# Kernel optimization log

Hardware: AMD Instinct MI355X
Metric: run time of the kernel (lower is better)

Reference implementation:

```python
import jax, jax.numpy as jnp
import numpy as np

N_NODES = 100000
N_EDGES = 1600000
N_GRAPHS = 128
IN_DIM, HID, OUT_DIM, DOC_DIM = 64, 128, 32, 768
LAYERS = 3


def setup_inputs() -> dict:
    key = jax.random.key(0)
    ks = jax.random.split(key, 24)
    s = 0.05
    inp = {
        "x": jax.random.normal(ks[0], (N_NODES, IN_DIM), jnp.float32),
        "doc_features": jax.random.normal(ks[1], (N_GRAPHS, DOC_DIM), jnp.float32),
        "edge_index": jax.random.randint(ks[2], (2, N_EDGES), 0, N_NODES, jnp.int64),
        "batch": jnp.sort(jax.random.randint(ks[3], (N_NODES,), 0, N_GRAPHS, jnp.int64)),
        # parameters (stored as [in, out] so y = x @ W + b)
        "node_w": jax.random.normal(ks[4], (IN_DIM, HID), jnp.float32) * s,
        "node_b": jnp.zeros((HID,), jnp.float32),
        "ggnn_w": jax.random.normal(ks[5], (LAYERS, HID, HID), jnp.float32) * s,
        "gru_w_ih": jax.random.normal(ks[6], (HID, 3 * HID), jnp.float32) * s,
        "gru_b_ih": jnp.zeros((3 * HID,), jnp.float32),
        "gru_w_hh": jax.random.normal(ks[7], (HID, 3 * HID), jnp.float32) * s,
        "gru_b_hh": jnp.zeros((3 * HID,), jnp.float32),
        "doc_w": jax.random.normal(ks[8], (DOC_DIM, HID), jnp.float32) * s,
        "doc_b": jnp.zeros((HID,), jnp.float32),
        "ln_g": jnp.ones((2 * HID,), jnp.float32),
        "ln_b": jnp.zeros((2 * HID,), jnp.float32),
        "fus_w": jax.random.normal(ks[9], (2 * HID, HID), jnp.float32) * s,
        "fus_b": jnp.zeros((HID,), jnp.float32),
        "task_w": jax.random.normal(ks[10], (HID, OUT_DIM), jnp.float32) * s,
        "task_b": jnp.zeros((OUT_DIM,), jnp.float32),
        "time_w": jax.random.normal(ks[11], (HID, 1), jnp.float32) * s,
        "time_b": jnp.zeros((1,), jnp.float32),
    }
    return inp


def _gru(m, h, w_ih, b_ih, w_hh, b_hh):
    gi = m @ w_ih + b_ih  # [N, 3H]
    gh = h @ w_hh + b_hh
    ir, iz, in_ = jnp.split(gi, 3, axis=-1)
    hr, hz, hn = jnp.split(gh, 3, axis=-1)
    r = jax.nn.sigmoid(ir + hr)
    z = jax.nn.sigmoid(iz + hz)
    n = jnp.tanh(in_ + r * hn)
    return (1.0 - z) * n + z * h


def reference(x, doc_features, node_w, node_b, ggnn_w, gru_w_ih, gru_b_ih,
              gru_w_hh, gru_b_hh, doc_w, doc_b, ln_g, ln_b, fus_w, fus_b,
              task_w, task_b, time_w, time_b, edge_index, batch):
    N = x.shape[0]
    src, dst = edge_index[0], edge_index[1]
    # node projection + ReLU
    h = jax.nn.relu(x @ node_w + node_b)  # [N, H]
    # GatedGraphConv: 3 layers of (linear -> scatter-add over edges -> GRU)
    for i in range(LAYERS):
        m = h @ ggnn_w[i]                              # [N, H]
        agg = jax.ops.segment_sum(m[src], dst, num_segments=N)  # scatter-add
        h = _gru(agg, h, gru_w_ih, gru_b_ih, gru_w_hh, gru_b_hh)
    # global mean pool over graphs
    sums = jax.ops.segment_sum(h, batch, num_segments=N_GRAPHS)  # [G, H]
    cnt = jax.ops.segment_sum(jnp.ones((N,), h.dtype), batch, num_segments=N_GRAPHS)
    pooled = sums / jnp.maximum(cnt, 1.0)[:, None]
    # doc projection + fusion head
    doc_emb = jax.nn.relu(doc_features @ doc_w + doc_b)  # [G, H]
    fusion = jnp.concatenate([pooled, doc_emb], axis=1)  # [G, 2H]
    mu = jnp.mean(fusion, axis=-1, keepdims=True)
    var = jnp.mean(jnp.square(fusion - mu), axis=-1, keepdims=True)
    fusion = (fusion - mu) * jax.lax.rsqrt(var + 1e-5) * ln_g + ln_b
    fusion = jax.nn.relu(fusion @ fus_w + fus_b)  # dropout is identity (eval)
    task_output = fusion @ task_w + task_b
    time_output = fusion @ time_w + time_b
    return (task_output, time_output)
```

## Files before the change

### kernel.cpp

```cpp
#include <hip/hip_runtime.h>

#define N_NODES  100000
#define N_EDGES  1600000
#define N_GRAPHS 128

#define BSH      8
#define BNODES   (1 << BSH)
#define NBUCK    391
#define NBLK_P1  512
#define EPB      (N_EDGES / NBLK_P1)
#define BKT_SCAN_N   (NBUCK * NBLK_P1)
#define SCAN_BLK_BKT 196
#define SCAN_BLK_NODE 98

typedef unsigned short u16;
typedef unsigned int   u32;
typedef __attribute__((ext_vector_type(8))) short short8;
typedef __attribute__((ext_vector_type(4))) float f32x4;

__device__ __forceinline__ float bf2f(u16 v) {
  union { u32 i; float f; } u; u.i = ((u32)v) << 16; return u.f;
}
__device__ __forceinline__ u16 f2bf(float f) {
  union { float f; u32 i; } u; u.f = f;
  u32 r = (u.i + 0x7fffu + ((u.i >> 16) & 1u)) >> 16;
  return (u16)r;
}
__device__ __forceinline__ float sigmoid_f(float x) { return 1.f / (1.f + __expf(-x)); }
__device__ __forceinline__ float tanh_f(float x) {
  x = fminf(15.f, fmaxf(-15.f, x));
  float e = __expf(2.f * x);
  return (e - 1.f) / (e + 1.f);
}
__device__ __forceinline__ int geti(const int* __restrict__ p, int i, int is64) {
  return p[is64 ? (2 * i) : i];
}

__global__ void detect_i64_kernel(const int* __restrict__ ei, const int* __restrict__ batch,
                                  int* __restrict__ flags) {
  int lane = threadIdx.x;
  {
    long long q = (long long)lane * (3200000 / 2 - 1) / 63;
    int pos = (int)(2 * q + 1);
    unsigned long long m = __ballot(ei[pos] != 0);
    if (lane == 0) flags[0] = (m == 0ull) ? 1 : 0;
  }
  {
    long long q = (long long)lane * (100000 / 2 - 1) / 63;
    int pos = (int)(2 * q + 1);
    unsigned long long m = __ballot(batch[pos] != 0);
    if (lane == 0) flags[1] = (m == 0ull) ? 1 : 0;
  }
}


__global__ __launch_bounds__(256)
void bucket_hist(const int* __restrict__ ei, const int* __restrict__ flags,
                 int* __restrict__ bcounts) {
  __shared__ int h[NBUCK];
  const int f = flags[0];
  for (int b = threadIdx.x; b < NBUCK; b += 256) h[b] = 0;
  __syncthreads();
  const int e0 = blockIdx.x * EPB;
  for (int i = threadIdx.x; i < EPB; i += 256) {
    int d = geti(ei, N_EDGES + e0 + i, f);
    atomicAdd(&h[d >> BSH], 1);
  }
  __syncthreads();
  for (int b = threadIdx.x; b < NBUCK; b += 256)
    bcounts[b * NBLK_P1 + blockIdx.x] = h[b];
}

__global__ __launch_bounds__(256)
void bucket_scatter(const int* __restrict__ ei, const int* __restrict__ flags,
                    const int* __restrict__ bbases, u32* __restrict__ bedges) {
  __shared__ int cur[NBUCK];
  const int f = flags[0];
  for (int b = threadIdx.x; b < NBUCK; b += 256)
    cur[b] = bbases[b * NBLK_P1 + blockIdx.x];
  __syncthreads();
  const int e0 = blockIdx.x * EPB;
  for (int i = threadIdx.x; i < EPB; i += 256) {
    int e = e0 + i;
    int d = geti(ei, N_EDGES + e, f);
    int s = geti(ei, e, f);
    int pos = atomicAdd(&cur[d >> BSH], 1);
    bedges[pos] = ((u32)(d & (BNODES - 1)) << 17) | (u32)s;
  }
}

__global__ __launch_bounds__(256)
void node_count(const u32* __restrict__ bedges, const int* __restrict__ bbases,
                int* __restrict__ counts) {
  __shared__ int h[BNODES];
  const int b = blockIdx.x;
  for (int i = threadIdx.x; i < BNODES; i += 256) h[i] = 0;
  __syncthreads();
  const int beg = bbases[b * NBLK_P1];
  const int end = (b + 1 < NBUCK) ? bbases[(b + 1) * NBLK_P1] : N_EDGES;
  for (int e = beg + threadIdx.x; e < end; e += 256)
    atomicAdd(&h[bedges[e] >> 17], 1);
  __syncthreads();
  const int node0 = b << BSH;
  for (int i = threadIdx.x; i < BNODES; i += 256)
    if (node0 + i < N_NODES) counts[node0 + i] = h[i];
}

__global__ __launch_bounds__(256)
void final_scatter(const u32* __restrict__ bedges, const int* __restrict__ bbases,
                   const int* __restrict__ offs, int* __restrict__ ssrc) {
  __shared__ int cur[BNODES];
  const int b = blockIdx.x;
  const int node0 = b << BSH;
  for (int i = threadIdx.x; i < BNODES; i += 256)
    cur[i] = (node0 + i < N_NODES) ? offs[node0 + i] : 0;
  __syncthreads();
  const int beg = bbases[b * NBLK_P1];
  const int end = (b + 1 < NBUCK) ? bbases[(b + 1) * NBLK_P1] : N_EDGES;
  for (int e = beg + threadIdx.x; e < end; e += 256) {
    u32 v = bedges[e];
    int pos = atomicAdd(&cur[v >> 17], 1);
    ssrc[pos] = (int)(v & 0x1FFFFu);
  }
}

__global__ __launch_bounds__(1024)
void scanA_kernel(const int* __restrict__ counts, int n, int* __restrict__ blocksums) {
  __shared__ int red[16];
  int i = blockIdx.x * 1024 + threadIdx.x;
  int v = (i < n) ? counts[i] : 0;
  for (int o = 32; o > 0; o >>= 1) v += __shfl_down(v, o, 64);
  int wv = threadIdx.x >> 6, lane = threadIdx.x & 63;
  if (lane == 0) red[wv] = v;
  __syncthreads();
  if (threadIdx.x < 16) {
    int s = red[threadIdx.x];
    for (int o = 8; o > 0; o >>= 1) s += __shfl_down(s, o, 64);
    if (threadIdx.x == 0) blocksums[blockIdx.x] = s;
  }
}

__global__ void scanB_kernel(const int* __restrict__ blocksums, int nblocks,
                             int* __restrict__ blockbase, int* __restrict__ total_out) {
  if (threadIdx.x == 0) {
    int run = 0;
    for (int b = 0; b < nblocks; ++b) { blockbase[b] = run; run += blocksums[b]; }
    if (total_out) *total_out = run;
  }
}

__global__ __launch_bounds__(1024)
void scanC_kernel(const int* __restrict__ counts, int n, const int* __restrict__ blockbase,
                  int* __restrict__ offsets) {
  __shared__ int buf[1024];
  int t = threadIdx.x;
  int i = blockIdx.x * 1024 + t;
  int v = (i < n) ? counts[i] : 0;
  buf[t] = v;
  __syncthreads();
  for (int o = 1; o < 1024; o <<= 1) {
    int add = (t >= o) ? buf[t - o] : 0;
    __syncthreads();
    buf[t] += add;
    __syncthreads();
  }
  if (i < n) offsets[i] = buf[t] - v + blockbase[blockIdx.x];
}

__global__ void transpose_kernel(const float* __restrict__ in, u16* __restrict__ out, int K, int N) {
  int i = blockIdx.x * 256 + threadIdx.x;
  if (i < K * N) {
    int k = i / N, n = i % N;
    out[n * K + k] = f2bf(in[i]);
  }
}

__global__ void wprime_kernel(const float* __restrict__ ggnn_w, const float* __restrict__ w_ih,
                              float* __restrict__ wp) {
  int i = blockIdx.x * 256 + threadIdx.x;
  if (i >= 3 * 128 * 384) return;
  int l = i / (128 * 384), r = i % (128 * 384), k = r / 384, c = r % 384;
  const float* W = ggnn_w + l * 128 * 128;
  float s = 0.f;
  for (int j = 0; j < 128; ++j) s += W[k * 128 + j] * w_ih[j * 384 + c];
  wp[i] = s;
}

__global__ void build_b2q_kernel(const float* __restrict__ wp, const float* __restrict__ w_hh,
                                 u16* __restrict__ b2q) {
  int g = blockIdx.x * 256 + threadIdx.x;
  if (g >= 98304) return;
  int r = g;
  int e    = r & 7;  r >>= 3;
  int col  = r & 15; r >>= 4;
  int quad = r & 3;  r >>= 2;
  int gate = r % 3;  r /= 3;
  int ci4  = r & 3;  r >>= 2;
  int half = r & 1;  r >>= 1;
  int oc   = r;
  int k = half * 128 + ci4 * 32 + quad * 8 + e;
  int n_lin = gate * 128 + oc * 16 + col;
  float v = (k < 128) ? wp[k * 384 + n_lin] : w_hh[(k - 128) * 384 + n_lin];
  b2q[g] = f2bf(v);
}

__global__ __launch_bounds__(256)
void nodeproj_gemm(const float* __restrict__ A, const u16* __restrict__ BT,
                   const float* __restrict__ bias, u16* __restrict__ out, int M)
{
  constexpr int K_DIM = 64, N_DIM = 128, NT = 8, NCHUNK = 2;
  __shared__ u16 B_lds[N_DIM * 40];
  const int tid = threadIdx.x, lane = tid & 63, w = tid >> 6;
  const int strip = blockIdx.x * 64;
  const int ksub = (lane >> 4) * 8;
  union Frag { uint4 u; short8 s; };
  Frag af[NCHUNK];
  const int m_node = strip + w * 16 + (lane & 15);
  const bool avalid = (m_node < M);
#pragma unroll
  for (int ci = 0; ci < NCHUNK; ++ci) {
    int k0 = ci * 32 + ksub;
    short8 sv = {0,0,0,0,0,0,0,0};
    if (avalid) {
      const float* p = A + (size_t)m_node * K_DIM + k0;
      float4 f0 = *(const float4*)p;
      float4 f1 = *(const float4*)(p + 4);
      sv[0]=(short)f2bf(f0.x); sv[1]=(short)f2bf(f0.y); sv[2]=(short)f2bf(f0.z); sv[3]=(short)f2bf(f0.w);
      sv[4]=(short)f2bf(f1.x); sv[5]=(short)f2bf(f1.y); sv[6]=(short)f2bf(f1.z); sv[7]=(short)f2bf(f1.w);
    }
    af[ci].s = sv;
  }
  f32x4 acc[NT];
#pragma unroll
  for (int t = 0; t < NT; ++t) acc[t] = {0.f, 0.f, 0.f, 0.f};
  const int boff = (lane & 15) * 40 + ksub;
#pragma unroll
  for (int ci = 0; ci < NCHUNK; ++ci) {
    if (ci) __syncthreads();
    for (int g = tid; g < N_DIM * 4; g += 256) {
      int n = g >> 2, ko = g & 3;
      uint4 bv = *(const uint4*)(BT + (size_t)n * K_DIM + ci * 32 + ko * 8);
      *(uint4*)(&B_lds[n * 40 + ko * 8]) = bv;
    }
    __syncthreads();
    short8 a = af[ci].s;
#pragma unroll
    for (int t = 0; t < NT; ++t) {
      const short8 b = *(const short8*)(&B_lds[t * 16 * 40 + boff]);
      acc[t] = __builtin_amdgcn_mfma_f32_16x16x32_bf16(a, b, acc[t], 0, 0, 0);
    }
  }
  const int mrow = (lane >> 4) * 4;
#pragma unroll
  for (int t = 0; t < NT; ++t) {
    int col = t * 16 + (lane & 15);
    float bv = bias[col];
#pragma unroll
    for (int r = 0; r < 4; ++r) {
      int node = strip + w * 16 + mrow + r;
      if (node < M) out[(size_t)node * N_DIM + col] = f2bf(fmaxf(acc[t][r] + bv, 0.f));
    }
  }
}

__global__ __launch_bounds__(256, 6)
void gru_gemm(const u16* __restrict__ agg, const u16* __restrict__ h,
              const u16* __restrict__ b2q, const float* __restrict__ b_ih,
              const float* __restrict__ b_hh, u16* __restrict__ hout, int M)
{
  __shared__ u16 Blds[12288];
  const int tid  = threadIdx.x;
  const int lane = tid & 63;
  const int w    = tid >> 6;
  const int bid  = blockIdx.x;
  const int xcd = bid & 7, idx = bid >> 3;
  const int linear = ((xcd < 4) ? xcd * 782 : 4 * 782 + (xcd - 4) * 781) + idx;
  const int op    = linear & 3;
  const int strip = (linear >> 2) * 64;
  const int lrow = lane & 15;
  const int quad = lane >> 4;

  const int node = strip + w * 16 + lrow;
  const bool nv = (node < M);
  const u16* qsrc0 = b2q + (size_t)(op * 2)     * 12288;
  const u16* qsrc1 = b2q + (size_t)(op * 2 + 1) * 12288;

  union Frag { uint4 u; short8 s8; };
  Frag a[2];
  const uint4 zz = {0u, 0u, 0u, 0u};
  auto lda = [&](int ci, int p) {
    const u16* ap = (ci < 4) ? (agg + ci * 32 + quad * 8) : (h + (ci - 4) * 32 + quad * 8);
    a[p].u = nv ? *(const uint4*)(ap + (size_t)node * 128) : zz;
  };

  lda(0, 0);
  lda(1, 1);
  for (int i2 = tid; i2 < 768; i2 += 256) {
    *(uint4*)(&Blds[i2 * 8])        = *(const uint4*)(qsrc0 + i2 * 8);
    *(uint4*)(&Blds[6144 + i2 * 8]) = *(const uint4*)(qsrc1 + i2 * 8);
  }

  f32x4 ar[2], az[2], ain[2], ahn[2];
#pragma unroll
  for (int t = 0; t < 2; ++t) {
    ar[t] = {0.f,0.f,0.f,0.f}; az[t] = {0.f,0.f,0.f,0.f};
    ain[t] = {0.f,0.f,0.f,0.f}; ahn[t] = {0.f,0.f,0.f,0.f};
  }

  __syncthreads();

#pragma unroll
  for (int ci = 0; ci < 8; ++ci) {
    if (ci == 4) {
      __syncthreads();
      for (int i2 = tid; i2 < 768; i2 += 256) {
        *(uint4*)(&Blds[i2 * 8])        = *(const uint4*)(qsrc0 + 6144 + i2 * 8);
        *(uint4*)(&Blds[6144 + i2 * 8]) = *(const uint4*)(qsrc1 + 6144 + i2 * 8);
      }
      __syncthreads();
    }
    const int p = ci & 1;
    short8 A = a[p].s8;
    if (ci < 6) lda(ci + 2, p);
#pragma unroll
    for (int t = 0; t < 2; ++t) {
      const u16* lb = &Blds[t * 6144 + (ci & 3) * 1536 + quad * 128 + lrow * 8];
      short8 br = *(const short8*)(lb);
      short8 bz = *(const short8*)(lb + 512);
      short8 bg = *(const short8*)(lb + 1024);
      ar[t] = __builtin_amdgcn_mfma_f32_16x16x32_bf16(A, br, ar[t], 0, 0, 0);
      az[t] = __builtin_amdgcn_mfma_f32_16x16x32_bf16(A, bz, az[t], 0, 0, 0);
      if (ci < 4) ain[t] = __builtin_amdgcn_mfma_f32_16x16x32_bf16(A, bg, ain[t], 0, 0, 0);
      else        ahn[t] = __builtin_amdgcn_mfma_f32_16x16x32_bf16(A, bg, ahn[t], 0, 0, 0);
    }
  }

  __syncthreads();
  u16* Olds = (u16*)Blds;
#pragma unroll
  for (int t = 0; t < 2; ++t) {
    const int c = op * 32 + t * 16 + lrow;
    const float brr = b_ih[c] + b_hh[c];
    const float bzz = b_ih[128 + c] + b_hh[128 + c];
    const float bin = b_ih[256 + c];
    const float bhn = b_hh[256 + c];
#pragma unroll
    for (int r = 0; r < 4; ++r) {
      const int lr   = w * 16 + quad * 4 + r;
      const int nrow = strip + lr;
      u16 val = 0;
      if (nrow < M) {
        float rg = sigmoid_f(ar[t][r] + brr);
        float zg = sigmoid_f(az[t][r] + bzz);
        float hv = ahn[t][r] + bhn;
        float ng = tanh_f(ain[t][r] + bin + rg * hv);
        float hp = bf2f(h[(size_t)nrow * 128 + c]);
        val = f2bf((1.f - zg) * ng + zg * hp);
      }
      Olds[lr * 32 + t * 16 + lrow] = val;
    }
  }
  __syncthreads();
  {
    const int row = tid >> 2, c4 = tid & 3;
    const int nrow = strip + row;
    if (nrow < M)
      *(uint4*)(&hout[(size_t)nrow * 128 + op * 32 + c4 * 8]) =
          *(const uint4*)(&Olds[row * 32 + c4 * 8]);
  }
}

__global__ __launch_bounds__(256)
void agg_kernel(const u16* __restrict__ m, const int* __restrict__ ssrc,
                const int* __restrict__ offsets, u16* __restrict__ agg)
{
  int node = blockIdx.x * 4 + (threadIdx.x >> 6);
  int lane = threadIdx.x & 63;
  if (node >= N_NODES) return;
  const int g = lane >> 4, l = lane & 15;
  int beg = offsets[node], end = offsets[node + 1];
  float s[8] = {0.f,0.f,0.f,0.f,0.f,0.f,0.f,0.f};
  for (int e = beg; e < end; e += 16) {
    uint4 v0 = {0u,0u,0u,0u}, v1 = {0u,0u,0u,0u};
    uint4 v2 = {0u,0u,0u,0u}, v3 = {0u,0u,0u,0u};
    int e0 = e + g, e1 = e + 4 + g, e2 = e + 8 + g, e3 = e + 12 + g;
    if (e0 < end) { int src = ssrc[e0]; v0 = *(const uint4*)(m + (size_t)src * 128 + l * 8); }
    if (e1 < end) { int src = ssrc[e1]; v1 = *(const uint4*)(m + (size_t)src * 128 + l * 8); }
    if (e2 < end) { int src = ssrc[e2]; v2 = *(const uint4*)(m + (size_t)src * 128 + l * 8); }
    if (e3 < end) { int src = ssrc[e3]; v3 = *(const uint4*)(m + (size_t)src * 128 + l * 8); }
    u32 w0[4] = {v0.x, v0.y, v0.z, v0.w};
    u32 w1[4] = {v1.x, v1.y, v1.z, v1.w};
    u32 w2[4] = {v2.x, v2.y, v2.z, v2.w};
    u32 w3[4] = {v3.x, v3.y, v3.z, v3.w};
#pragma unroll
    for (int i = 0; i < 4; ++i) {
      s[2*i]   += (bf2f((u16)(w0[i] & 0xffffu)) + bf2f((u16)(w1[i] & 0xffffu)))
                + (bf2f((u16)(w2[i] & 0xffffu)) + bf2f((u16)(w3[i] & 0xffffu)));
      s[2*i+1] += (bf2f((u16)(w0[i] >> 16))     + bf2f((u16)(w1[i] >> 16)))
                + (bf2f((u16)(w2[i] >> 16))     + bf2f((u16)(w3[i] >> 16)));
    }
  }
#pragma unroll
  for (int i = 0; i < 8; ++i) {
    s[i] += __shfl_xor(s[i], 16, 64);
    s[i] += __shfl_xor(s[i], 32, 64);
  }
  if (g == 0) {
    uint4 o;
    o.x = (u32)f2bf(s[0]) | ((u32)f2bf(s[1]) << 16);
    o.y = (u32)f2bf(s[2]) | ((u32)f2bf(s[3]) << 16);
    o.z = (u32)f2bf(s[4]) | ((u32)f2bf(s[5]) << 16);
    o.w = (u32)f2bf(s[6]) | ((u32)f2bf(s[7]) << 16);
    *(uint4*)(agg + (size_t)node * 128 + l * 8) = o;
  }
}

__global__ __launch_bounds__(256)
void pool_kernel(const u16* __restrict__ h, const int* __restrict__ batch,
                 const int* __restrict__ flags, float* __restrict__ sums)
{
  const int c = threadIdx.x & 127;
  const int half = threadIdx.x >> 7;
  const int base = blockIdx.x * 128;
  const int f = flags[1];
  int gcur = -1; float s = 0.f;
  for (int i = half; i < 128; i += 2) {
    int n = base + i;
    if (n >= N_NODES) break;
    int g = geti(batch, n, f);
    if (g != gcur) {
      if (gcur >= 0) atomicAdd(&sums[gcur * 128 + c], s);
      s = 0.f; gcur = g;
    }
    s += bf2f(h[(size_t)n * 128 + c]);
  }
  if (gcur >= 0) atomicAdd(&sums[gcur * 128 + c], s);
}

__global__ __launch_bounds__(256)
void head2_kernel(const float* __restrict__ sums, const int* __restrict__ batch,
                  const int* __restrict__ flags,
                  const float* __restrict__ doc, const float* __restrict__ doc_w, const float* __restrict__ doc_b,
                  const float* __restrict__ ln_g, const float* __restrict__ ln_b,
                  const float* __restrict__ fus_w, const float* __restrict__ fus_b,
                  const float* __restrict__ task_w, const float* __restrict__ task_b,
                  const float* __restrict__ time_w, const float* __restrict__ time_b,
                  float* __restrict__ out_task, float* __restrict__ out_time)
{
  const int g = blockIdx.x;
  const int t = threadIdx.x;
  __shared__ float fusion[256];
  __shared__ float fh[128];
  __shared__ float dpart[256];
  __shared__ int seg[2];

  if (t < 2) {
    int f = flags[1];
    int target = g + t, lo = 0, hi = N_NODES;
    while (lo < hi) { int mid = (lo + hi) >> 1; if (geti(batch, mid, f) < target) lo = mid + 1; else hi = mid; }
    seg[t] = lo;
  }
  {
    int c = t & 127, kh = t >> 7;
    float s = 0.f;
    for (int k = kh * 384; k < kh * 384 + 384; ++k) s += doc[g * 768 + k] * doc_w[k * 128 + c];
    dpart[t] = s;
  }
  __syncthreads();

  if (t < 128) {
    float cnt = (float)(seg[1] - seg[0]);
    fusion[t] = sums[g * 128 + t] / fmaxf(cnt, 1.f);
  } else {
    int c = t - 128;
    fusion[t] = fmaxf(dpart[c] + dpart[c + 128] + doc_b[c], 0.f);
  }
  __syncthreads();

  float mu = 0.f;
  for (int i = 0; i < 256; ++i) mu += fusion[i];
  mu *= (1.f / 256.f);
  float var = 0.f;
  for (int i = 0; i < 256; ++i) { float d = fusion[i] - mu; var += d * d; }
  var *= (1.f / 256.f);
  float inv = rsqrtf(var + 1e-5f);
  float norm = (fusion[t] - mu) * inv * ln_g[t] + ln_b[t];
  __syncthreads();
  fusion[t] = norm;
  __syncthreads();

  if (t < 128) {
    float s = 0.f;
    for (int k = 0; k < 256; ++k) s += fusion[k] * fus_w[k * 128 + t];
    s += fus_b[t];
    fh[t] = fmaxf(s, 0.f);
  }
  __syncthreads();

  if (t < 32) {
    float s = 0.f;
    for (int k = 0; k < 128; ++k) s += fh[k] * task_w[k * 32 + t];
    s += task_b[t];
    out_task[g * 32 + t] = s;
  }
  if (t == 32) {
    float s = 0.f;
    for (int k = 0; k < 128; ++k) s += fh[k] * time_w[k];
    s += time_b[0];
    out_time[g] = s;
  }
}

extern "C" void kernel_launch(void* const* d_in, const int* in_sizes, int n_in,
                              void* d_out, int out_size, void* d_ws, size_t ws_size,
                              hipStream_t stream)
{
  const float* x        = (const float*)d_in[0];
  const float* doc      = (const float*)d_in[1];
  const int*   ei       = (const int*)d_in[2];
  const int*   batch    = (const int*)d_in[3];
  const float* node_w   = (const float*)d_in[4];
  const float* node_b   = (const float*)d_in[5];
  const float* ggnn_w   = (const float*)d_in[6];
  const float* gru_w_ih = (const float*)d_in[7];
  const float* gru_b_ih = (const float*)d_in[8];
  const float* gru_w_hh = (const float*)d_in[9];
  const float* gru_b_hh = (const float*)d_in[10];
  const float* doc_w    = (const float*)d_in[11];
  const float* doc_b    = (const float*)d_in[12];
  const float* ln_g     = (const float*)d_in[13];
  const float* ln_b     = (const float*)d_in[14];
  const float* fus_w    = (const float*)d_in[15];
  const float* fus_b    = (const float*)d_in[16];
  const float* task_w   = (const float*)d_in[17];
  const float* task_b   = (const float*)d_in[18];
  const float* time_w   = (const float*)d_in[19];
  const float* time_b   = (const float*)d_in[20];

  char* ws = (char*)d_ws;
  size_t off = 0;
  auto alloc = [&](size_t bytes) -> void* {
    void* p = ws + off;
    off = (off + bytes + 255) & ~(size_t)255;
    return p;
  };
  u16* aggb    = (u16*)alloc((size_t)N_NODES * 128 * 2);
  u16* hA      = (u16*)alloc((size_t)N_NODES * 128 * 2);
  u16* hB      = (u16*)alloc((size_t)N_NODES * 128 * 2);
  u16* nwT     = (u16*)alloc(64 * 128 * 2);
  u16* b2q     = (u16*)alloc(3 * 98304 * 2);
  float* wp    = (float*)alloc(3 * 128 * 384 * 4);
  float* sums  = (float*)alloc(N_GRAPHS * 128 * 4);
  int* counts  = (int*)alloc((size_t)N_NODES * 4);
  int* offs    = (int*)alloc((size_t)(N_NODES + 1) * 4);
  int* ssrc    = (int*)alloc((size_t)N_EDGES * 4);
  int* bsum    = (int*)alloc(SCAN_BLK_BKT * 4);
  int* bbase   = (int*)alloc(SCAN_BLK_BKT * 4);
  int* flags   = (int*)alloc(2 * 4);

  u32* bedges  = (u32*)aggb;
  int* bcounts = (int*)((char*)aggb + 6400000);
  int* bbases  = (int*)((char*)aggb + 7200768);

  hipMemsetAsync(sums, 0, (size_t)N_GRAPHS * 128 * 4, stream);

  detect_i64_kernel<<<1, 64, 0, stream>>>(ei, batch, flags);

  bucket_hist<<<NBLK_P1, 256, 0, stream>>>(ei, flags, bcounts);
  scanA_kernel<<<SCAN_BLK_BKT, 1024, 0, stream>>>(bcounts, BKT_SCAN_N, bsum);
  scanB_kernel<<<1, 64, 0, stream>>>(bsum, SCAN_BLK_BKT, bbase, (int*)nullptr);
  scanC_kernel<<<SCAN_BLK_BKT, 1024, 0, stream>>>(bcounts, BKT_SCAN_N, bbase, bbases);
  bucket_scatter<<<NBLK_P1, 256, 0, stream>>>(ei, flags, bbases, bedges);
  node_count<<<NBUCK, 256, 0, stream>>>(bedges, bbases, counts);
  scanA_kernel<<<SCAN_BLK_NODE, 1024, 0, stream>>>(counts, N_NODES, bsum);
  scanB_kernel<<<1, 64, 0, stream>>>(bsum, SCAN_BLK_NODE, bbase, offs + N_NODES);
  scanC_kernel<<<SCAN_BLK_NODE, 1024, 0, stream>>>(counts, N_NODES, bbase, offs);
  final_scatter<<<NBUCK, 256, 0, stream>>>(bedges, bbases, offs, ssrc);

  transpose_kernel<<<(64 * 128 + 255) / 256, 256, 0, stream>>>(node_w, nwT, 64, 128);
  wprime_kernel<<<(3 * 128 * 384 + 255) / 256, 256, 0, stream>>>(ggnn_w, gru_w_ih, wp);
  for (int l = 0; l < 3; ++l)
    build_b2q_kernel<<<(98304 + 255) / 256, 256, 0, stream>>>(
        wp + l * 128 * 384, gru_w_hh, b2q + (size_t)l * 98304);

  const int GB = (N_NODES + 63) / 64;
  const int GBGRU = ((N_NODES + 63) / 64) * 4;
  nodeproj_gemm<<<GB, 256, 0, stream>>>(x, nwT, node_b, hA, N_NODES);

  u16* hcur = hA;
  u16* hnext = hB;
  for (int l = 0; l < 3; ++l) {
    agg_kernel<<<(N_NODES + 3) / 4, 256, 0, stream>>>(hcur, ssrc, offs, aggb);
    gru_gemm<<<GBGRU, 256, 0, stream>>>(aggb, hcur, b2q + (size_t)l * 98304,
                                        gru_b_ih, gru_b_hh, hnext, N_NODES);
    u16* tmp = hcur; hcur = hnext; hnext = tmp;
  }

  pool_kernel<<<(N_NODES + 127) / 128, 256, 0, stream>>>(hcur, batch, flags, sums);

  float* out_task = (float*)d_out;
  float* out_time = out_task + N_GRAPHS * 32;
  head2_kernel<<<N_GRAPHS, 256, 0, stream>>>(sums, batch, flags, doc, doc_w, doc_b, ln_g, ln_b,
                                             fus_w, fus_b, task_w, task_b, time_w, time_b,
                                             out_task, out_time);
}
```

Baseline: 620.8 us.

## Fuse edge aggregation into GRU GEMM with LDS-resident aggregates and double-buffered weights

Merges the separate gather/scatter-add kernel and the GRU GEMM into one kernel per layer. Each 512-thread block first aggregates neighbour features for its 64 nodes into a swizzled LDS tile, then runs the GRU GEMM across all 384 output columns using double-buffered weight chunks staged from a reordered B layout. This removes the global round trip of the aggregate tensor and one launch per layer. In exchange each block now recomputes nothing but loses the 4-way column split, which lowers grid parallelism and puts the irregular gather and the MFMA phase in sequence inside the same block, with higher LDS use that may limit occupancy.

```diff
diff --git a/kernel.cpp b/kernel.cpp
--- a/kernel.cpp
+++ b/kernel.cpp
@@ -191,15 +191,13 @@
   int g = blockIdx.x * 256 + threadIdx.x;
   if (g >= 98304) return;
   int r = g;
-  int e    = r & 7;  r >>= 3;
-  int col  = r & 15; r >>= 4;
-  int quad = r & 3;  r >>= 2;
-  int gate = r % 3;  r /= 3;
-  int ci4  = r & 3;  r >>= 2;
-  int half = r & 1;  r >>= 1;
-  int oc   = r;
-  int k = half * 128 + ci4 * 32 + quad * 8 + e;
-  int n_lin = gate * 128 + oc * 16 + col;
+  int e    = r & 7;   r >>= 3;
+  int col  = r & 127; r >>= 7;
+  int quad = r & 3;   r >>= 2;
+  int gate = r % 3;   r /= 3;
+  int ci   = r;
+  int k = ci * 32 + quad * 8 + e;
+  int n_lin = gate * 128 + col;
   float v = (k < 128) ? wp[k * 384 + n_lin] : w_hh[(k - 128) * 384 + n_lin];
   b2q[g] = f2bf(v);
 }
@@ -263,46 +261,91 @@
   }
 }
 
-__global__ __launch_bounds__(256, 6)
-void gru_gemm(const u16* __restrict__ agg, const u16* __restrict__ h,
-              const u16* __restrict__ b2q, const float* __restrict__ b_ih,
-              const float* __restrict__ b_hh, u16* __restrict__ hout, int M)
+__global__ __launch_bounds__(512, 4)
+void fused_layer(const u16* __restrict__ h, const int* __restrict__ ssrc,
+                 const int* __restrict__ offsets, const u16* __restrict__ b2q,
+                 const float* __restrict__ b_ih, const float* __restrict__ b_hh,
+                 u16* __restrict__ hout, int M)
 {
-  __shared__ u16 Blds[12288];
+  __shared__ u16 aggT[8192];
+  __shared__ u16 Bbuf[2][12288];
   const int tid  = threadIdx.x;
   const int lane = tid & 63;
   const int w    = tid >> 6;
-  const int bid  = blockIdx.x;
-  const int xcd = bid & 7, idx = bid >> 3;
-  const int linear = ((xcd < 4) ? xcd * 782 : 4 * 782 + (xcd - 4) * 781) + idx;
-  const int op    = linear & 3;
-  const int strip = (linear >> 2) * 64;
+  const int strip = blockIdx.x * 64;
+  const int rw   = (w & 3) * 16;
+  const int ch   = w >> 2;
   const int lrow = lane & 15;
   const int quad = lane >> 4;
 
-  const int node = strip + w * 16 + lrow;
-  const bool nv = (node < M);
-  const u16* qsrc0 = b2q + (size_t)(op * 2)     * 12288;
-  const u16* qsrc1 = b2q + (size_t)(op * 2 + 1) * 12288;
+  {
+    const int g4 = lane >> 4, l16 = lane & 15;
+    for (int i = 0; i < 8; ++i) {
+      const int nl = w * 8 + i;
+      const int n  = strip + nl;
+      float s[8] = {0.f,0.f,0.f,0.f,0.f,0.f,0.f,0.f};
+      if (n < M) {
+        int beg = offsets[n], end = offsets[n + 1];
+        for (int e = beg; e < end; e += 16) {
+          uint4 v0 = {0u,0u,0u,0u}, v1 = {0u,0u,0u,0u};
+          uint4 v2 = {0u,0u,0u,0u}, v3 = {0u,0u,0u,0u};
+          int e0 = e + g4, e1 = e + 4 + g4, e2 = e + 8 + g4, e3 = e + 12 + g4;
+          if (e0 < end) { int sv = ssrc[e0]; v0 = *(const uint4*)(h + (size_t)sv * 128 + l16 * 8); }
+          if (e1 < end) { int sv = ssrc[e1]; v1 = *(const uint4*)(h + (size_t)sv * 128 + l16 * 8); }
+          if (e2 < end) { int sv = ssrc[e2]; v2 = *(const uint4*)(h + (size_t)sv * 128 + l16 * 8); }
+          if (e3 < end) { int sv = ssrc[e3]; v3 = *(const uint4*)(h + (size_t)sv * 128 + l16 * 8); }
+          u32 w0[4] = {v0.x, v0.y, v0.z, v0.w};
+          u32 w1[4] = {v1.x, v1.y, v1.z, v1.w};
+          u32 w2[4] = {v2.x, v2.y, v2.z, v2.w};
+          u32 w3[4] = {v3.x, v3.y, v3.z, v3.w};
+#pragma unroll
+          for (int q = 0; q < 4; ++q) {
+            s[2*q]   += (bf2f((u16)(w0[q] & 0xffffu)) + bf2f((u16)(w1[q] & 0xffffu)))
+                      + (bf2f((u16)(w2[q] & 0xffffu)) + bf2f((u16)(w3[q] & 0xffffu)));
+            s[2*q+1] += (bf2f((u16)(w0[q] >> 16))     + bf2f((u16)(w1[q] >> 16)))
+                      + (bf2f((u16)(w2[q] >> 16))     + bf2f((u16)(w3[q] >> 16)));
+          }
+        }
+      }
+#pragma unroll
+      for (int q = 0; q < 8; ++q) {
+        s[q] += __shfl_xor(s[q], 16, 64);
+        s[q] += __shfl_xor(s[q], 32, 64);
+      }
+      if (g4 == 0) {
+        uint4 o;
+        o.x = (u32)f2bf(s[0]) | ((u32)f2bf(s[1]) << 16);
+        o.y = (u32)f2bf(s[2]) | ((u32)f2bf(s[3]) << 16);
+        o.z = (u32)f2bf(s[4]) | ((u32)f2bf(s[5]) << 16);
+        o.w = (u32)f2bf(s[6]) | ((u32)f2bf(s[7]) << 16);
+        int idx = (nl * 128 + l16 * 8) ^ ((nl & 7) << 3);
+        *(uint4*)(&aggT[idx]) = o;
+      }
+    }
+  }
 
   union Frag { uint4 u; short8 s8; };
-  Frag a[2];
+  const int arow = strip + rw + lrow;
+  const bool av = (arow < M);
   const uint4 zz = {0u, 0u, 0u, 0u};
-  auto lda = [&](int ci, int p) {
-    const u16* ap = (ci < 4) ? (agg + ci * 32 + quad * 8) : (h + (ci - 4) * 32 + quad * 8);
-    a[p].u = nv ? *(const uint4*)(ap + (size_t)node * 128) : zz;
+  Frag ha[4];
+#pragma unroll
+  for (int c = 0; c < 4; ++c)
+    ha[c].u = av ? *(const uint4*)(h + (size_t)arow * 128 + c * 32 + quad * 8) : zz;
+
+  auto stageB = [&](int ci, int buf) {
+    const u16* src = b2q + (size_t)ci * 12288;
+#pragma unroll
+    for (int k = 0; k < 3; ++k) {
+      int idx = tid + k * 512;
+      *(uint4*)(&Bbuf[buf][idx * 8]) = *(const uint4*)(src + idx * 8);
+    }
   };
-
-  lda(0, 0);
-  lda(1, 1);
-  for (int i2 = tid; i2 < 768; i2 += 256) {
-    *(uint4*)(&Blds[i2 * 8])        = *(const uint4*)(qsrc0 + i2 * 8);
-    *(uint4*)(&Blds[6144 + i2 * 8]) = *(const uint4*)(qsrc1 + i2 * 8);
-  }
-
-  f32x4 ar[2], az[2], ain[2], ahn[2];
-#pragma unroll
-  for (int t = 0; t < 2; ++t) {
+  stageB(0, 0);
+
+  f32x4 ar[4], az[4], ain[4], ahn[4];
+#pragma unroll
+  for (int t = 0; t < 4; ++t) {
     ar[t] = {0.f,0.f,0.f,0.f}; az[t] = {0.f,0.f,0.f,0.f};
     ain[t] = {0.f,0.f,0.f,0.f}; ahn[t] = {0.f,0.f,0.f,0.f};
   }
@@ -311,42 +354,40 @@
 
 #pragma unroll
   for (int ci = 0; ci < 8; ++ci) {
-    if (ci == 4) {
-      __syncthreads();
-      for (int i2 = tid; i2 < 768; i2 += 256) {
-        *(uint4*)(&Blds[i2 * 8])        = *(const uint4*)(qsrc0 + 6144 + i2 * 8);
-        *(uint4*)(&Blds[6144 + i2 * 8]) = *(const uint4*)(qsrc1 + 6144 + i2 * 8);
-      }
-      __syncthreads();
-    }
     const int p = ci & 1;
-    short8 A = a[p].s8;
-    if (ci < 6) lda(ci + 2, p);
-#pragma unroll
-    for (int t = 0; t < 2; ++t) {
-      const u16* lb = &Blds[t * 6144 + (ci & 3) * 1536 + quad * 128 + lrow * 8];
+    if (ci < 7) stageB(ci + 1, p ^ 1);
+    short8 A;
+    if (ci < 4) {
+      const int row = rw + lrow;
+      const int idx = (row * 128 + ci * 32 + quad * 8) ^ ((row & 7) << 3);
+      A = *(const short8*)(&aggT[idx]);
+    } else {
+      A = ha[ci - 4].s8;
+    }
+#pragma unroll
+    for (int t = 0; t < 4; ++t) {
+      const u16* lb = &Bbuf[p][quad * 1024 + (ch * 64 + t * 16 + lrow) * 8];
       short8 br = *(const short8*)(lb);
-      short8 bz = *(const short8*)(lb + 512);
-      short8 bg = *(const short8*)(lb + 1024);
+      short8 bz = *(const short8*)(lb + 4096);
+      short8 bg = *(const short8*)(lb + 8192);
       ar[t] = __builtin_amdgcn_mfma_f32_16x16x32_bf16(A, br, ar[t], 0, 0, 0);
       az[t] = __builtin_amdgcn_mfma_f32_16x16x32_bf16(A, bz, az[t], 0, 0, 0);
       if (ci < 4) ain[t] = __builtin_amdgcn_mfma_f32_16x16x32_bf16(A, bg, ain[t], 0, 0, 0);
       else        ahn[t] = __builtin_amdgcn_mfma_f32_16x16x32_bf16(A, bg, ahn[t], 0, 0, 0);
     }
-  }
-
-  __syncthreads();
-  u16* Olds = (u16*)Blds;
-#pragma unroll
-  for (int t = 0; t < 2; ++t) {
-    const int c = op * 32 + t * 16 + lrow;
+    __syncthreads();
+  }
+
+#pragma unroll
+  for (int t = 0; t < 4; ++t) {
+    const int c = ch * 64 + t * 16 + lrow;
     const float brr = b_ih[c] + b_hh[c];
     const float bzz = b_ih[128 + c] + b_hh[128 + c];
     const float bin = b_ih[256 + c];
     const float bhn = b_hh[256 + c];
 #pragma unroll
     for (int r = 0; r < 4; ++r) {
-      const int lr   = w * 16 + quad * 4 + r;
+      const int lr   = rw + quad * 4 + r;
       const int nrow = strip + lr;
       u16 val = 0;
       if (nrow < M) {
@@ -357,61 +398,19 @@
         float hp = bf2f(h[(size_t)nrow * 128 + c]);
         val = f2bf((1.f - zg) * ng + zg * hp);
       }
-      Olds[lr * 32 + t * 16 + lrow] = val;
-    }
-  }
-  __syncthreads();
-  {
-    const int row = tid >> 2, c4 = tid & 3;
+      aggT[(lr * 128 + c) ^ ((lr & 7) << 3)] = val;
+    }
+  }
+  __syncthreads();
+#pragma unroll
+  for (int rr = 0; rr < 2; ++rr) {
+    const int row = (tid >> 4) + rr * 32;
+    const int c16 = tid & 15;
     const int nrow = strip + row;
-    if (nrow < M)
-      *(uint4*)(&hout[(size_t)nrow * 128 + op * 32 + c4 * 8]) =
-          *(const uint4*)(&Olds[row * 32 + c4 * 8]);
-  }
-}
-
-__global__ __launch_bounds__(256)
-void agg_kernel(const u16* __restrict__ m, const int* __restrict__ ssrc,
-                const int* __restrict__ offsets, u16* __restrict__ agg)
-{
-  int node = blockIdx.x * 4 + (threadIdx.x >> 6);
-  int lane = threadIdx.x & 63;
-  if (node >= N_NODES) return;
-  const int g = lane >> 4, l = lane & 15;
-  int beg = offsets[node], end = offsets[node + 1];
-  float s[8] = {0.f,0.f,0.f,0.f,0.f,0.f,0.f,0.f};
-  for (int e = beg; e < end; e += 16) {
-    uint4 v0 = {0u,0u,0u,0u}, v1 = {0u,0u,0u,0u};
-    uint4 v2 = {0u,0u,0u,0u}, v3 = {0u,0u,0u,0u};
-    int e0 = e + g, e1 = e + 4 + g, e2 = e + 8 + g, e3 = e + 12 + g;
-    if (e0 < end) { int src = ssrc[e0]; v0 = *(const uint4*)(m + (size_t)src * 128 + l * 8); }
-    if (e1 < end) { int src = ssrc[e1]; v1 = *(const uint4*)(m + (size_t)src * 128 + l * 8); }
-    if (e2 < end) { int src = ssrc[e2]; v2 = *(const uint4*)(m + (size_t)src * 128 + l * 8); }
-    if (e3 < end) { int src = ssrc[e3]; v3 = *(const uint4*)(m + (size_t)src * 128 + l * 8); }
-    u32 w0[4] = {v0.x, v0.y, v0.z, v0.w};
-    u32 w1[4] = {v1.x, v1.y, v1.z, v1.w};
-    u32 w2[4] = {v2.x, v2.y, v2.z, v2.w};
-    u32 w3[4] = {v3.x, v3.y, v3.z, v3.w};
-#pragma unroll
-    for (int i = 0; i < 4; ++i) {
-      s[2*i]   += (bf2f((u16)(w0[i] & 0xffffu)) + bf2f((u16)(w1[i] & 0xffffu)))
-                + (bf2f((u16)(w2[i] & 0xffffu)) + bf2f((u16)(w3[i] & 0xffffu)));
-      s[2*i+1] += (bf2f((u16)(w0[i] >> 16))     + bf2f((u16)(w1[i] >> 16)))
-                + (bf2f((u16)(w2[i] >> 16))     + bf2f((u16)(w3[i] >> 16)));
-    }
-  }
-#pragma unroll
-  for (int i = 0; i < 8; ++i) {
-    s[i] += __shfl_xor(s[i], 16, 64);
-    s[i] += __shfl_xor(s[i], 32, 64);
-  }
-  if (g == 0) {
-    uint4 o;
-    o.x = (u32)f2bf(s[0]) | ((u32)f2bf(s[1]) << 16);
-    o.y = (u32)f2bf(s[2]) | ((u32)f2bf(s[3]) << 16);
-    o.z = (u32)f2bf(s[4]) | ((u32)f2bf(s[5]) << 16);
-    o.w = (u32)f2bf(s[6]) | ((u32)f2bf(s[7]) << 16);
-    *(uint4*)(agg + (size_t)node * 128 + l * 8) = o;
+    if (nrow < M) {
+      const int idx = (row * 128 + c16 * 8) ^ ((row & 7) << 3);
+      *(uint4*)(&hout[(size_t)nrow * 128 + c16 * 8]) = *(const uint4*)(&aggT[idx]);
+    }
   }
 }
 
@@ -584,14 +583,12 @@
         wp + l * 128 * 384, gru_w_hh, b2q + (size_t)l * 98304);
 
   const int GB = (N_NODES + 63) / 64;
-  const int GBGRU = ((N_NODES + 63) / 64) * 4;
   nodeproj_gemm<<<GB, 256, 0, stream>>>(x, nwT, node_b, hA, N_NODES);
 
   u16* hcur = hA;
   u16* hnext = hB;
   for (int l = 0; l < 3; ++l) {
-    agg_kernel<<<(N_NODES + 3) / 4, 256, 0, stream>>>(hcur, ssrc, offs, aggb);
-    gru_gemm<<<GBGRU, 256, 0, stream>>>(aggb, hcur, b2q + (size_t)l * 98304,
+    fused_layer<<<GB, 512, 0, stream>>>(hcur, ssrc, offs, b2q + (size_t)l * 98304,
                                         gru_b_ih, gru_b_hh, hnext, N_NODES);
     u16* tmp = hcur; hcur = hnext; hnext = tmp;
   }
```

New measurement: 700.1 us. 12.8% more time.

## Widen GRU GEMM blocks to 512 threads covering half the output columns

Applied to the files above, without the earlier changes.

The GRU GEMM now tiles 64 rows by 64 output columns per 512-thread block (two column chunks instead of four). A fragments for each node strip are therefore loaded by half as many blocks, cutting redundant global reads of agg and h. The B-weight layout is rebuilt to match, and the LDS tile doubles to 48KB. The risk is lower occupancy per CU and a larger staging cost per block.

```diff
diff --git a/kernel.cpp b/kernel.cpp
--- a/kernel.cpp
+++ b/kernel.cpp
@@ -191,15 +191,13 @@
   int g = blockIdx.x * 256 + threadIdx.x;
   if (g >= 98304) return;
   int r = g;
-  int e    = r & 7;  r >>= 3;
-  int col  = r & 15; r >>= 4;
-  int quad = r & 3;  r >>= 2;
-  int gate = r % 3;  r /= 3;
-  int ci4  = r & 3;  r >>= 2;
-  int half = r & 1;  r >>= 1;
-  int oc   = r;
-  int k = half * 128 + ci4 * 32 + quad * 8 + e;
-  int n_lin = gate * 128 + oc * 16 + col;
+  int e    = r & 7;   r >>= 3;
+  int col  = r & 127; r >>= 7;
+  int quad = r & 3;   r >>= 2;
+  int gate = r % 3;   r /= 3;
+  int ci   = r;
+  int k = ci * 32 + quad * 8 + e;
+  int n_lin = gate * 128 + col;
   float v = (k < 128) ? wp[k * 384 + n_lin] : w_hh[(k - 128) * 384 + n_lin];
   b2q[g] = f2bf(v);
 }
@@ -263,27 +261,27 @@
   }
 }
 
-__global__ __launch_bounds__(256, 6)
+__global__ __launch_bounds__(512, 6)
 void gru_gemm(const u16* __restrict__ agg, const u16* __restrict__ h,
               const u16* __restrict__ b2q, const float* __restrict__ b_ih,
               const float* __restrict__ b_hh, u16* __restrict__ hout, int M)
 {
-  __shared__ u16 Blds[12288];
+  __shared__ u16 Blds[24576];
   const int tid  = threadIdx.x;
   const int lane = tid & 63;
   const int w    = tid >> 6;
   const int bid  = blockIdx.x;
   const int xcd = bid & 7, idx = bid >> 3;
-  const int linear = ((xcd < 4) ? xcd * 782 : 4 * 782 + (xcd - 4) * 781) + idx;
-  const int op    = linear & 3;
-  const int strip = (linear >> 2) * 64;
+  const int linear = ((xcd < 6) ? xcd * 391 : 6 * 391 + (xcd - 6) * 390) + idx;
+  const int ch2  = linear & 1;
+  const int strip = (linear >> 1) * 64;
+  const int rw   = (w & 3) * 16;
+  const int cb   = (w >> 2) * 32;
   const int lrow = lane & 15;
   const int quad = lane >> 4;
 
-  const int node = strip + w * 16 + lrow;
+  const int node = strip + rw + lrow;
   const bool nv = (node < M);
-  const u16* qsrc0 = b2q + (size_t)(op * 2)     * 12288;
-  const u16* qsrc1 = b2q + (size_t)(op * 2 + 1) * 12288;
 
   union Frag { uint4 u; short8 s8; };
   Frag a[2];
@@ -293,12 +291,22 @@
     a[p].u = nv ? *(const uint4*)(ap + (size_t)node * 128) : zz;
   };
 
+  auto stageB = [&](int half) {
+#pragma unroll
+    for (int k = 0; k < 6; ++k) {
+      const int i4  = tid + k * 512;
+      const int run = i4 >> 6, off = i4 & 63;
+      const int ci  = run / 12, rem = run - ci * 12;
+      const int gt  = rem >> 2, qd = rem & 3;
+      const size_t so = (size_t)(half * 4 + ci) * 12288 + gt * 4096 + qd * 1024
+                        + ch2 * 512 + off * 8;
+      *(uint4*)(&Blds[run * 512 + off * 8]) = *(const uint4*)(b2q + so);
+    }
+  };
+
   lda(0, 0);
   lda(1, 1);
-  for (int i2 = tid; i2 < 768; i2 += 256) {
-    *(uint4*)(&Blds[i2 * 8])        = *(const uint4*)(qsrc0 + i2 * 8);
-    *(uint4*)(&Blds[6144 + i2 * 8]) = *(const uint4*)(qsrc1 + i2 * 8);
-  }
+  stageB(0);
 
   f32x4 ar[2], az[2], ain[2], ahn[2];
 #pragma unroll
@@ -313,10 +321,7 @@
   for (int ci = 0; ci < 8; ++ci) {
     if (ci == 4) {
       __syncthreads();
-      for (int i2 = tid; i2 < 768; i2 += 256) {
-        *(uint4*)(&Blds[i2 * 8])        = *(const uint4*)(qsrc0 + 6144 + i2 * 8);
-        *(uint4*)(&Blds[6144 + i2 * 8]) = *(const uint4*)(qsrc1 + 6144 + i2 * 8);
-      }
+      stageB(1);
       __syncthreads();
     }
     const int p = ci & 1;
@@ -324,10 +329,10 @@
     if (ci < 6) lda(ci + 2, p);
 #pragma unroll
     for (int t = 0; t < 2; ++t) {
-      const u16* lb = &Blds[t * 6144 + (ci & 3) * 1536 + quad * 128 + lrow * 8];
+      const u16* lb = &Blds[(ci & 3) * 6144 + quad * 512 + (cb + t * 16 + lrow) * 8];
       short8 br = *(const short8*)(lb);
-      short8 bz = *(const short8*)(lb + 512);
-      short8 bg = *(const short8*)(lb + 1024);
+      short8 bz = *(const short8*)(lb + 2048);
+      short8 bg = *(const short8*)(lb + 4096);
       ar[t] = __builtin_amdgcn_mfma_f32_16x16x32_bf16(A, br, ar[t], 0, 0, 0);
       az[t] = __builtin_amdgcn_mfma_f32_16x16x32_bf16(A, bz, az[t], 0, 0, 0);
       if (ci < 4) ain[t] = __builtin_amdgcn_mfma_f32_16x16x32_bf16(A, bg, ain[t], 0, 0, 0);
@@ -339,14 +344,15 @@
   u16* Olds = (u16*)Blds;
 #pragma unroll
   for (int t = 0; t < 2; ++t) {
-    const int c = op * 32 + t * 16 + lrow;
+    const int cl = cb + t * 16 + lrow;
+    const int c  = ch2 * 64 + cl;
     const float brr = b_ih[c] + b_hh[c];
     const float bzz = b_ih[128 + c] + b_hh[128 + c];
     const float bin = b_ih[256 + c];
     const float bhn = b_hh[256 + c];
 #pragma unroll
     for (int r = 0; r < 4; ++r) {
-      const int lr   = w * 16 + quad * 4 + r;
+      const int lr   = rw + quad * 4 + r;
       const int nrow = strip + lr;
       u16 val = 0;
       if (nrow < M) {
@@ -357,16 +363,16 @@
         float hp = bf2f(h[(size_t)nrow * 128 + c]);
         val = f2bf((1.f - zg) * ng + zg * hp);
       }
-      Olds[lr * 32 + t * 16 + lrow] = val;
+      Olds[lr * 64 + cl] = val;
     }
   }
   __syncthreads();
   {
-    const int row = tid >> 2, c4 = tid & 3;
+    const int row = tid >> 3, c8 = tid & 7;
     const int nrow = strip + row;
     if (nrow < M)
-      *(uint4*)(&hout[(size_t)nrow * 128 + op * 32 + c4 * 8]) =
-          *(const uint4*)(&Olds[row * 32 + c4 * 8]);
+      *(uint4*)(&hout[(size_t)nrow * 128 + ch2 * 64 + c8 * 8]) =
+          *(const uint4*)(&Olds[row * 64 + c8 * 8]);
   }
 }
 
@@ -584,14 +590,14 @@
         wp + l * 128 * 384, gru_w_hh, b2q + (size_t)l * 98304);
 
   const int GB = (N_NODES + 63) / 64;
-  const int GBGRU = ((N_NODES + 63) / 64) * 4;
+  const int GBGRU = ((N_NODES + 63) / 64) * 2;
   nodeproj_gemm<<<GB, 256, 0, stream>>>(x, nwT, node_b, hA, N_NODES);
 
   u16* hcur = hA;
   u16* hnext = hB;
   for (int l = 0; l < 3; ++l) {
     agg_kernel<<<(N_NODES + 3) / 4, 256, 0, stream>>>(hcur, ssrc, offs, aggb);
-    gru_gemm<<<GBGRU, 256, 0, stream>>>(aggb, hcur, b2q + (size_t)l * 98304,
+    gru_gemm<<<GBGRU, 512, 0, stream>>>(aggb, hcur, b2q + (size_t)l * 98304,
                                         gru_b_ih, gru_b_hh, hnext, N_NODES);
     u16* tmp = hcur; hcur = hnext; hnext = tmp;
   }
```

Result: no change. 627.4 us (+1.1%).
